# Optimization experiments

Hardware: AMD Instinct MI355X
Metric: run time of the kernel (lower is better)

## Reference

```python
import jax, jax.numpy as jnp
import numpy as np

B, T, F, L, H, O = 32, 12, 4, 1024, 64, 1  # batch, time, features, links, hidden, target features


def setup_inputs() -> dict:
    key = jax.random.key(0)
    ks = jax.random.split(key, 16)
    stdv = 1.0 / np.sqrt(H)
    u = lambda k, shape: jax.random.uniform(k, shape, jnp.float32, -stdv, stdv)
    # adjacency/attention: diagonal 1, immediate neighbors alpha=0.2 (chain road network)
    attention = jnp.eye(L, dtype=jnp.float32) \
        + 0.2 * jnp.eye(L, k=1, dtype=jnp.float32) \
        + 0.2 * jnp.eye(L, k=-1, dtype=jnp.float32)
    x = jax.random.normal(ks[0], (B, T, F, L), jnp.float32)
    return dict(
        x=x,
        attention=attention,          # [L, L] (all partitions' rows concatenated)
        w_rh=u(ks[1], (L, H, H)), b_rh=u(ks[2], (H, L)),
        w_ri=u(ks[3], (L, F, H)), b_ri=u(ks[4], (H, L)),
        w_uh=u(ks[5], (L, H, H)), b_uh=u(ks[6], (H, L)),
        w_ui=u(ks[7], (L, F, H)), b_ui=u(ks[8], (H, L)),
        w_nh=u(ks[9], (L, H, H)), b_nh=u(ks[10], (H, L)),
        w_ni=u(ks[11], (L, F, H)), b_ni=u(ks[12], (H, L)),
        w_fc=u(ks[13], (L, H, O)), b_fc=u(ks[14], (O, L)),
    )


def reference(x, attention, w_rh, b_rh, w_ri, b_ri, w_uh, b_uh, w_ui, b_ui,
              w_nh, b_nh, w_ni, b_ni, w_fc, b_fc):
    # x: [B, T, F, L]; hidden: [B, H, L]
    def step(h, xt):
        # graph attention: each link attends over its neighbors' hidden states
        hatt = jnp.einsum('bhl,pl->bhp', h, attention)  # [B, H, L]
        # per-link batched matmuls for gates
        r = jax.nn.sigmoid(
            jnp.einsum('bhl,lhk->bkl', hatt, w_rh) + b_rh[None]
            + jnp.einsum('bfl,lfk->bkl', xt, w_ri) + b_ri[None])
        z = jax.nn.sigmoid(
            jnp.einsum('bhl,lhk->bkl', hatt, w_uh) + b_uh[None]
            + jnp.einsum('bfl,lfk->bkl', xt, w_ui) + b_ui[None])
        n = jnp.tanh(
            jnp.einsum('bfl,lfk->bkl', xt, w_ni) + b_ni[None]
            + r * (jnp.einsum('bhl,lhk->bkl', hatt, w_nh) + b_nh[None]))
        h_new = (1.0 - z) * n + z * h
        return h_new, None

    h0 = jnp.zeros((B, H, L), x.dtype)
    xs = jnp.moveaxis(x, 1, 0)  # [T, B, F, L]
    hT, _ = jax.lax.scan(step, h0, xs)
    # per-link fully connected output head
    out = jnp.einsum('bhl,lht->btl', hT, w_fc) + b_fc[None]  # [B, O, L]
    return out
```

## Files before the change

### kernel.cpp

```cpp
#include <hip/hip_runtime.h>

#define B_ 32
#define T_ 12
#define F_ 4
#define L_ 1024
#define H_ 64
#define NROWS 1920
#define NCH 256
#define CONE 8
#define MARG 2

typedef _Float16 f16x8 __attribute__((ext_vector_type(8)));
typedef float f32x4 __attribute__((ext_vector_type(4)));
typedef unsigned long long u64;

#define MFMA __builtin_amdgcn_mfma_f32_16x16x32_f16

__device__ __forceinline__ int chunk_of_block(int bid) {
    return ((bid & 7) << 5) + (bid >> 3);
}
__device__ __forceinline__ int clampi(int v, int lo, int hi) {
    return v < lo ? lo : (v > hi ? hi : v);
}
__device__ __forceinline__ int h_byte(int p, int slot, int b, int k) {
    int byte = ((((p * CONE + slot) * 32 + b) * 64) + k) * 2;
    return byte ^ ((b & 7) << 4);
}

__global__ __launch_bounds__(256) void prep(
    const float* __restrict__ x,
    const float* __restrict__ b_rh, const float* __restrict__ b_ri,
    const float* __restrict__ b_uh, const float* __restrict__ b_ui,
    const float* __restrict__ b_nh, const float* __restrict__ b_ni,
    float* __restrict__ params)
{
    const int tid = threadIdx.x;
    const int rt  = blockIdx.x >> 4;
    const int lt  = blockIdx.x & 15;
    __shared__ float lds[64][65];

    #pragma unroll
    for (int i = 0; i < 16; ++i) {
        const int e  = i * 256 + tid;
        const int rl = e >> 6, ll = e & 63;
        const int r  = rt * 64 + rl, l = lt * 64 + ll;
        float v;
        if (r < 1536) {
            v = x[(size_t)r * L_ + l];
        } else {
            const int rb = r - 1536;
            const int g  = rb >> 6;
            const float* bp = (g == 0) ? b_rh : (g == 1) ? b_ri : (g == 2) ? b_uh
                            : (g == 3) ? b_ui : (g == 4) ? b_nh : b_ni;
            v = bp[(size_t)(rb & 63) * L_ + l];
        }
        lds[rl][ll] = v;
    }
    __syncthreads();
    #pragma unroll
    for (int i = 0; i < 16; ++i) {
        const int e  = i * 256 + tid;
        const int ll = e >> 6, rl = e & 63;
        params[(size_t)(lt * 64 + ll) * NROWS + rt * 64 + rl] = lds[rl][ll];
    }
}

__global__ __launch_bounds__(256) void prep_w(
    const float* __restrict__ w_rh, const float* __restrict__ w_uh,
    const float* __restrict__ w_nh,
    const float* __restrict__ w_ri, const float* __restrict__ w_ui,
    const float* __restrict__ w_ni,
    const float* __restrict__ b_rh, const float* __restrict__ b_ri,
    const float* __restrict__ b_uh, const float* __restrict__ b_ui,
    const float* __restrict__ b_ni,
    _Float16* __restrict__ Wpk)
{
    const int l  = blockIdx.x;
    const int fq = threadIdx.x >> 6, m = threadIdx.x & 63;
    const int n  = m & 15, kq = m >> 4;
    #pragma unroll
    for (int i = 0; i < 9; ++i) {
        const int f  = i * 4 + fq;
        const int nt = f / 9, s = f % 9;
        const int grp = s / 3, sub = s % 3;
        const int kout = nt * 16 + n;
        f16x8 v;
        if (sub < 2) {
            const float* wh = (grp == 0) ? w_rh : (grp == 1) ? w_uh : w_nh;
            #pragma unroll
            for (int j = 0; j < 8; ++j)
                v[j] = (_Float16)wh[(size_t)l * 4096
                         + (size_t)(sub * 32 + kq * 8 + j) * 64 + kout];
        } else {
            const float* wx = (grp == 0) ? w_ri : (grp == 1) ? w_ui : w_ni;
            float bias;
            if (grp == 0)      bias = b_rh[(size_t)kout * L_ + l] + b_ri[(size_t)kout * L_ + l];
            else if (grp == 1) bias = b_uh[(size_t)kout * L_ + l] + b_ui[(size_t)kout * L_ + l];
            else               bias = b_ni[(size_t)kout * L_ + l];
            #pragma unroll
            for (int j = 0; j < 8; ++j) {
                const int k = kq * 8 + j;
                v[j] = (k < 4) ? (_Float16)wx[(size_t)l * 256 + k * 64 + kout]
                     : (k == 4) ? (_Float16)bias
                                : (_Float16)0.0f;
            }
        }
        *(f16x8*)(Wpk + (((size_t)l * 36 + f) * 64 + m) * 8) = v;
    }
}

__global__ __launch_bounds__(512, 1) void gru_cone(
    const _Float16* __restrict__ Wpk,
    const float* __restrict__ att,  const float* __restrict__ params,
    const float* __restrict__ w_fc, const float* __restrict__ b_fc,
    float* __restrict__ out)
{
    const int c    = chunk_of_block(blockIdx.x);
    const int tid  = threadIdx.x;
    const int w    = tid >> 6, lane = tid & 63;
    const int n    = lane & 15, kq = lane >> 4;
    const int nth  = w & 1;
    const int clb  = w >> 1;
    const int base = 4 * c - MARG;

    __shared__ __align__(16) _Float16 hbuf[2 * CONE * 32 * 64];
    __shared__ __align__(16) _Float16 xls[CONE][1536];
    __shared__ float psum[4][2][B_];

    #pragma unroll
    for (int i = 0; i < 24; ++i) {
        const int e  = i * 512 + tid;
        const int cl = e / 1536, rem = e % 1536;
        const int gl = clampi(base + cl, 0, L_ - 1);
        xls[cl][rem] = (_Float16)params[(size_t)gl * NROWS + rem];
    }
    #pragma unroll
    for (int i = 0; i < 16; ++i)
        ((u64*)hbuf)[i * 512 + tid] = 0ull;

    bool     tval[2];
    _Float16 ach[2], alh[2], arh[2];
    float    bnh[2][2][4];
    f16x8    xw[2][2][3];
    #pragma unroll
    for (int j = 0; j < 2; ++j) {
        const int cl = clb + 4 * j;
        const int gl = base + cl;
        tval[j] = (gl >= 0 && gl < L_);
        const int glc = clampi(gl, 0, L_ - 1);
        ach[j] = tval[j] ? (_Float16)att[(size_t)glc * L_ + glc] : (_Float16)0.0f;
        alh[j] = (tval[j] && cl > 0 && gl > 0)
                   ? (_Float16)att[(size_t)glc * L_ + glc - 1] : (_Float16)0.0f;
        arh[j] = (tval[j] && cl < CONE - 1 && gl < L_ - 1)
                   ? (_Float16)att[(size_t)glc * L_ + glc + 1] : (_Float16)0.0f;
        const float* pb = params + (size_t)glc * NROWS + 1536;
        #pragma unroll
        for (int q = 0; q < 2; ++q) {
            #pragma unroll
            for (int r = 0; r < 4; ++r)
                bnh[j][q][r] = pb[256 + (nth * 2 + q) * 16 + kq * 4 + r];
            #pragma unroll
            for (int g = 0; g < 3; ++g)
                xw[j][q][g] = *(const f16x8*)(Wpk +
                    (((size_t)glc * 36 + (nth * 2 + q) * 9 + 2 + 3 * g) * 64 + lane) * 8);
        }
    }
    const int oidx = (clb < 2) ? clb + 2 : clb - 2;
    const int glo  = 4 * c + oidx;
    __syncthreads();

    #pragma unroll 1
    for (int t = 0; t < T_; ++t) {
        const int rp = t & 1, wpb = rp ^ 1;
        const int need = T_ - 1 - t;
        const char* hbr = (const char*)hbuf;
        char*       hbw = (char*)hbuf;

        #pragma unroll
        for (int j = 0; j < 2; ++j) {
            const int cl = clb + 4 * j;
            if (!tval[j]) continue;
            if (cl < 2 - need || cl > 5 + need) continue;
            const int gl = base + cl;
            const bool hid = (t > 0);

            f16x8 af[2][2];
            if (hid) {
                #pragma unroll
                for (int mt = 0; mt < 2; ++mt)
                    #pragma unroll
                    for (int ks = 0; ks < 2; ++ks) {
                        const int b = mt * 16 + n, k0 = ks * 32 + kq * 8;
                        const int sl = (cl > 0) ? cl - 1 : 0;
                        const int sr = (cl < CONE - 1) ? cl + 1 : CONE - 1;
                        const f16x8 hs = *(const f16x8*)(hbr + h_byte(rp, cl, b, k0));
                        const f16x8 hl = *(const f16x8*)(hbr + h_byte(rp, sl, b, k0));
                        const f16x8 hr = *(const f16x8*)(hbr + h_byte(rp, sr, b, k0));
                        af[mt][ks] = ach[j] * hs + alh[j] * hl + arh[j] * hr;
                    }
            }
            f16x8 ax[2] = {};
            if (kq == 0) {
                #pragma unroll
                for (int mt = 0; mt < 2; ++mt) {
                    #pragma unroll
                    for (int f = 0; f < 4; ++f)
                        ax[mt][f] = xls[cl][(mt * 16 + n) * 48 + t * 4 + f];
                    ax[mt][4] = (_Float16)1.0f;
                }
            }

            float sfc[2] = {0.0f, 0.0f};
            #pragma unroll
            for (int q = 0; q < 2; ++q) {
                const int kb = (nth * 2 + q) * 16 + kq * 4;
                const _Float16* wb = Wpk + (((size_t)gl * 36 + (nth * 2 + q) * 9) * 64) * 8;
                f32x4 ar[2] = {}, az[2] = {}, anh_[2] = {}, anx_[2] = {};
                if (hid) {
                    const f16x8 b0 = *(const f16x8*)(wb + (0 * 64 + lane) * 8);
                    const f16x8 b1 = *(const f16x8*)(wb + (1 * 64 + lane) * 8);
                    const f16x8 b3 = *(const f16x8*)(wb + (3 * 64 + lane) * 8);
                    const f16x8 b4 = *(const f16x8*)(wb + (4 * 64 + lane) * 8);
                    const f16x8 b6 = *(const f16x8*)(wb + (6 * 64 + lane) * 8);
                    const f16x8 b7 = *(const f16x8*)(wb + (7 * 64 + lane) * 8);
                    #pragma unroll
                    for (int mt = 0; mt < 2; ++mt) {
                        ar[mt]   = MFMA(b0, af[mt][0], ar[mt],   0, 0, 0);
                        ar[mt]   = MFMA(b1, af[mt][1], ar[mt],   0, 0, 0);
                        az[mt]   = MFMA(b3, af[mt][0], az[mt],   0, 0, 0);
                        az[mt]   = MFMA(b4, af[mt][1], az[mt],   0, 0, 0);
                        anh_[mt] = MFMA(b6, af[mt][0], anh_[mt], 0, 0, 0);
                        anh_[mt] = MFMA(b7, af[mt][1], anh_[mt], 0, 0, 0);
                    }
                }
                #pragma unroll
                for (int mt = 0; mt < 2; ++mt) {
                    ar[mt]   = MFMA(xw[j][q][0], ax[mt], ar[mt],   0, 0, 0);
                    az[mt]   = MFMA(xw[j][q][1], ax[mt], az[mt],   0, 0, 0);
                    anx_[mt] = MFMA(xw[j][q][2], ax[mt], anx_[mt], 0, 0, 0);
                }
                float4 wfc4;
                if (t == T_ - 1 && j == (clb < 2 ? 1 : 0))
                    wfc4 = *(const float4*)&w_fc[(size_t)glo * H_ + kb];
                #pragma unroll
                for (int mt = 0; mt < 2; ++mt) {
                    const int b = mt * 16 + n;
                    union { u64 u; _Float16 h[4]; } hp;
                    hp.u = hid ? *(const u64*)(hbr + h_byte(rp, cl, b, kb)) : 0ull;
                    union { u64 u; _Float16 h[4]; } hvp;
                    #pragma unroll
                    for (int r = 0; r < 4; ++r) {
                        const float pre_r = ar[mt][r];
                        const float pre_z = az[mt][r];
                        const float rg = __builtin_amdgcn_rcpf(1.0f + __expf(-pre_r));
                        const float zg = __builtin_amdgcn_rcpf(1.0f + __expf(-pre_z));
                        float npre = anx_[mt][r] + rg * (anh_[mt][r] + bnh[j][q][r]);
                        npre = fminf(fmaxf(npre, -15.0f), 15.0f);
                        const float e2 = __expf(2.0f * npre);
                        const float nn = (e2 - 1.0f) * __builtin_amdgcn_rcpf(e2 + 1.0f);
                        const float hv = (1.0f - zg) * nn + zg * (float)hp.h[r];
                        hvp.h[r] = (_Float16)hv;
                        if (t == T_ - 1) sfc[mt] += hv * (&wfc4.x)[r];
                    }
                    if (t < T_ - 1)
                        *(u64*)(hbw + h_byte(wpb, cl, b, kb)) = hvp.u;
                }
            }
            if (t == T_ - 1) {
                #pragma unroll
                for (int mt = 0; mt < 2; ++mt) {
                    float s = sfc[mt];
                    s += __shfl_xor(s, 16, 64);
                    s += __shfl_xor(s, 32, 64);
                    if (kq == 0) psum[oidx][nth][mt * 16 + n] = s;
                }
            }
        }
        __syncthreads();
    }

    if (tid < 128) {
        const int o = tid >> 5, b = tid & 31;
        const int gl = 4 * c + o;
        out[(size_t)b * L_ + gl] = psum[o][0][b] + psum[o][1][b] + b_fc[gl];
    }
}

extern "C" void kernel_launch(void* const* d_in, const int* in_sizes, int n_in,
                              void* d_out, int out_size, void* d_ws, size_t ws_size,
                              hipStream_t stream) {
    const float* x    = (const float*)d_in[0];
    const float* att  = (const float*)d_in[1];
    const float* w_rh = (const float*)d_in[2];
    const float* b_rh = (const float*)d_in[3];
    const float* w_ri = (const float*)d_in[4];
    const float* b_ri = (const float*)d_in[5];
    const float* w_uh = (const float*)d_in[6];
    const float* b_uh = (const float*)d_in[7];
    const float* w_ui = (const float*)d_in[8];
    const float* b_ui = (const float*)d_in[9];
    const float* w_nh = (const float*)d_in[10];
    const float* b_nh = (const float*)d_in[11];
    const float* w_ni = (const float*)d_in[12];
    const float* b_ni = (const float*)d_in[13];
    const float* w_fc = (const float*)d_in[14];
    const float* b_fc = (const float*)d_in[15];
    float* out = (float*)d_out;

    char* ws = (char*)d_ws;
    float*    params = (float*)ws;
    _Float16* Wpk    = (_Float16*)(ws + (8u << 20));

    prep<<<480, 256, 0, stream>>>(x, b_rh, b_ri, b_uh, b_ui, b_nh, b_ni, params);
    prep_w<<<L_, 256, 0, stream>>>(w_rh, w_uh, w_nh, w_ri, w_ui, w_ni,
                                   b_rh, b_ri, b_uh, b_ui, b_ni, Wpk);
    gru_cone<<<NCH, 512, 0, stream>>>(Wpk, att, params, w_fc, b_fc, out);
}
```

Measured before the change: 107.0 us.

## Use one wave pair per cone link and stage prep_w weights through LDS

The GRU cone kernel now launches 1024 threads, 16 waves, so each wave pair owns one of the eight cone links instead of looping over two links per wave. This doubles the parallelism per block and drops the per-wave j loop and its duplicated register state, at the cost of more waves competing for registers and the barrier. Separately, prep_w loads each link's three hidden weight matrices into shared memory with coalesced float4 reads before gathering the transposed f16 fragments, replacing strided global reads.

Result: slower. 163.1 us (+52.5%).

```diff
diff --git a/kernel.cpp b/kernel.cpp
--- a/kernel.cpp
+++ b/kernel.cpp
@@ -75,9 +75,30 @@
     const float* __restrict__ b_ni,
     _Float16* __restrict__ Wpk)
 {
-    const int l  = blockIdx.x;
-    const int fq = threadIdx.x >> 6, m = threadIdx.x & 63;
-    const int n  = m & 15, kq = m >> 4;
+    const int l   = blockIdx.x;
+    const int tid = threadIdx.x;
+    const int fq  = tid >> 6, m = tid & 63;
+    const int n   = m & 15, kq = m >> 4;
+
+    __shared__ float wst[3][64][65];
+
+    const float* whs[3] = { w_rh, w_uh, w_nh };
+    #pragma unroll
+    for (int g = 0; g < 3; ++g) {
+        const float4* src = (const float4*)(whs[g] + (size_t)l * 4096);
+        #pragma unroll
+        for (int i = 0; i < 4; ++i) {
+            const int e4 = i * 256 + tid;
+            const float4 v = src[e4];
+            const int row = e4 >> 4, col = (e4 & 15) * 4;
+            wst[g][row][col]     = v.x;
+            wst[g][row][col + 1] = v.y;
+            wst[g][row][col + 2] = v.z;
+            wst[g][row][col + 3] = v.w;
+        }
+    }
+    __syncthreads();
+
     #pragma unroll
     for (int i = 0; i < 9; ++i) {
         const int f  = i * 4 + fq;
@@ -86,11 +107,9 @@
         const int kout = nt * 16 + n;
         f16x8 v;
         if (sub < 2) {
-            const float* wh = (grp == 0) ? w_rh : (grp == 1) ? w_uh : w_nh;
             #pragma unroll
             for (int j = 0; j < 8; ++j)
-                v[j] = (_Float16)wh[(size_t)l * 4096
-                         + (size_t)(sub * 32 + kq * 8 + j) * 64 + kout];
+                v[j] = (_Float16)wst[grp][sub * 32 + kq * 8 + j][kout];
         } else {
             const float* wx = (grp == 0) ? w_ri : (grp == 1) ? w_ui : w_ni;
             float bias;
@@ -109,7 +128,7 @@
     }
 }
 
-__global__ __launch_bounds__(512, 1) void gru_cone(
+__global__ __launch_bounds__(1024, 1) void gru_cone(
     const _Float16* __restrict__ Wpk,
     const float* __restrict__ att,  const float* __restrict__ params,
     const float* __restrict__ w_fc, const float* __restrict__ b_fc,
@@ -120,7 +139,7 @@
     const int w    = tid >> 6, lane = tid & 63;
     const int n    = lane & 15, kq = lane >> 4;
     const int nth  = w & 1;
-    const int clb  = w >> 1;
+    const int cl   = w >> 1;
     const int base = 4 * c - MARG;
 
     __shared__ __align__(16) _Float16 hbuf[2 * CONE * 32 * 64];
@@ -128,45 +147,39 @@
     __shared__ float psum[4][2][B_];
 
     #pragma unroll
-    for (int i = 0; i < 24; ++i) {
-        const int e  = i * 512 + tid;
-        const int cl = e / 1536, rem = e % 1536;
-        const int gl = clampi(base + cl, 0, L_ - 1);
-        xls[cl][rem] = (_Float16)params[(size_t)gl * NROWS + rem];
-    }
-    #pragma unroll
-    for (int i = 0; i < 16; ++i)
-        ((u64*)hbuf)[i * 512 + tid] = 0ull;
-
-    bool     tval[2];
-    _Float16 ach[2], alh[2], arh[2];
-    float    bnh[2][2][4];
-    f16x8    xw[2][2][3];
-    #pragma unroll
-    for (int j = 0; j < 2; ++j) {
-        const int cl = clb + 4 * j;
-        const int gl = base + cl;
-        tval[j] = (gl >= 0 && gl < L_);
-        const int glc = clampi(gl, 0, L_ - 1);
-        ach[j] = tval[j] ? (_Float16)att[(size_t)glc * L_ + glc] : (_Float16)0.0f;
-        alh[j] = (tval[j] && cl > 0 && gl > 0)
-                   ? (_Float16)att[(size_t)glc * L_ + glc - 1] : (_Float16)0.0f;
-        arh[j] = (tval[j] && cl < CONE - 1 && gl < L_ - 1)
-                   ? (_Float16)att[(size_t)glc * L_ + glc + 1] : (_Float16)0.0f;
+    for (int i = 0; i < 12; ++i) {
+        const int e  = i * 1024 + tid;
+        const int sl = e / 1536, rem = e % 1536;
+        const int gl = clampi(base + sl, 0, L_ - 1);
+        xls[sl][rem] = (_Float16)params[(size_t)gl * NROWS + rem];
+    }
+    #pragma unroll
+    for (int i = 0; i < 8; ++i)
+        ((u64*)hbuf)[i * 1024 + tid] = 0ull;
+
+    const int  gl   = base + cl;
+    const bool tval = (gl >= 0 && gl < L_);
+    const int  glc  = clampi(gl, 0, L_ - 1);
+    const _Float16 ach = tval ? (_Float16)att[(size_t)glc * L_ + glc] : (_Float16)0.0f;
+    const _Float16 alh = (tval && cl > 0 && gl > 0)
+                           ? (_Float16)att[(size_t)glc * L_ + glc - 1] : (_Float16)0.0f;
+    const _Float16 arh = (tval && cl < CONE - 1 && gl < L_ - 1)
+                           ? (_Float16)att[(size_t)glc * L_ + glc + 1] : (_Float16)0.0f;
+    float bnh[2][4];
+    f16x8 xw[2][3];
+    {
         const float* pb = params + (size_t)glc * NROWS + 1536;
         #pragma unroll
         for (int q = 0; q < 2; ++q) {
             #pragma unroll
             for (int r = 0; r < 4; ++r)
-                bnh[j][q][r] = pb[256 + (nth * 2 + q) * 16 + kq * 4 + r];
+                bnh[q][r] = pb[256 + (nth * 2 + q) * 16 + kq * 4 + r];
             #pragma unroll
             for (int g = 0; g < 3; ++g)
-                xw[j][q][g] = *(const f16x8*)(Wpk +
+                xw[q][g] = *(const f16x8*)(Wpk +
                     (((size_t)glc * 36 + (nth * 2 + q) * 9 + 2 + 3 * g) * 64 + lane) * 8);
         }
     }
-    const int oidx = (clb < 2) ? clb + 2 : clb - 2;
-    const int glo  = 4 * c + oidx;
     __syncthreads();
 
     #pragma unroll 1
@@ -176,12 +189,7 @@
         const char* hbr = (const char*)hbuf;
         char*       hbw = (char*)hbuf;
 
-        #pragma unroll
-        for (int j = 0; j < 2; ++j) {
-            const int cl = clb + 4 * j;
-            if (!tval[j]) continue;
-            if (cl < 2 - need || cl > 5 + need) continue;
-            const int gl = base + cl;
+        if (tval && cl >= 2 - need && cl <= 5 + need) {
             const bool hid = (t > 0);
 
             f16x8 af[2][2];
@@ -196,7 +204,7 @@
                         const f16x8 hs = *(const f16x8*)(hbr + h_byte(rp, cl, b, k0));
                         const f16x8 hl = *(const f16x8*)(hbr + h_byte(rp, sl, b, k0));
                         const f16x8 hr = *(const f16x8*)(hbr + h_byte(rp, sr, b, k0));
-                        af[mt][ks] = ach[j] * hs + alh[j] * hl + arh[j] * hr;
+                        af[mt][ks] = ach * hs + alh * hl + arh * hr;
                     }
             }
             f16x8 ax[2] = {};
@@ -235,13 +243,13 @@
                 }
                 #pragma unroll
                 for (int mt = 0; mt < 2; ++mt) {
-                    ar[mt]   = MFMA(xw[j][q][0], ax[mt], ar[mt],   0, 0, 0);
-                    az[mt]   = MFMA(xw[j][q][1], ax[mt], az[mt],   0, 0, 0);
-                    anx_[mt] = MFMA(xw[j][q][2], ax[mt], anx_[mt], 0, 0, 0);
+                    ar[mt]   = MFMA(xw[q][0], ax[mt], ar[mt],   0, 0, 0);
+                    az[mt]   = MFMA(xw[q][1], ax[mt], az[mt],   0, 0, 0);
+                    anx_[mt] = MFMA(xw[q][2], ax[mt], anx_[mt], 0, 0, 0);
                 }
                 float4 wfc4;
-                if (t == T_ - 1 && j == (clb < 2 ? 1 : 0))
-                    wfc4 = *(const float4*)&w_fc[(size_t)glo * H_ + kb];
+                if (t == T_ - 1)
+                    wfc4 = *(const float4*)&w_fc[(size_t)gl * H_ + kb];
                 #pragma unroll
                 for (int mt = 0; mt < 2; ++mt) {
                     const int b = mt * 16 + n;
@@ -254,7 +262,7 @@
                         const float pre_z = az[mt][r];
                         const float rg = __builtin_amdgcn_rcpf(1.0f + __expf(-pre_r));
                         const float zg = __builtin_amdgcn_rcpf(1.0f + __expf(-pre_z));
-                        float npre = anx_[mt][r] + rg * (anh_[mt][r] + bnh[j][q][r]);
+                        float npre = anx_[mt][r] + rg * (anh_[mt][r] + bnh[q][r]);
                         npre = fminf(fmaxf(npre, -15.0f), 15.0f);
                         const float e2 = __expf(2.0f * npre);
                         const float nn = (e2 - 1.0f) * __builtin_amdgcn_rcpf(e2 + 1.0f);
@@ -272,7 +280,7 @@
                     float s = sfc[mt];
                     s += __shfl_xor(s, 16, 64);
                     s += __shfl_xor(s, 32, 64);
-                    if (kq == 0) psum[oidx][nth][mt * 16 + n] = s;
+                    if (kq == 0) psum[cl - 2][nth][mt * 16 + n] = s;
                 }
             }
         }
@@ -281,8 +289,8 @@
 
     if (tid < 128) {
         const int o = tid >> 5, b = tid & 31;
-        const int gl = 4 * c + o;
-        out[(size_t)b * L_ + gl] = psum[o][0][b] + psum[o][1][b] + b_fc[gl];
+        const int gl2 = 4 * c + o;
+        out[(size_t)b * L_ + gl2] = psum[o][0][b] + psum[o][1][b] + b_fc[gl2];
     }
 }
 
@@ -314,5 +322,5 @@
     prep<<<480, 256, 0, stream>>>(x, b_rh, b_ri, b_uh, b_ui, b_nh, b_ni, params);
     prep_w<<<L_, 256, 0, stream>>>(w_rh, w_uh, w_nh, w_ri, w_ui, w_ni,
                                    b_rh, b_ri, b_uh, b_ui, b_ni, Wpk);
-    gru_cone<<<NCH, 512, 0, stream>>>(Wpk, att, params, w_fc, b_fc, out);
-}
+    gru_cone<<<NCH, 1024, 0, stream>>>(Wpk, att, params, w_fc, b_fc, out);
+}
```

## Split batch across two blocks per chunk and stage recurrent weights in LDS

Applied to the files above, without the earlier changes.

The main GRU kernel now launches twice as many blocks, each handling 16 of the 32 batch rows for a chunk of links. This halves the per-block MFMA and LDS work and spreads it over more of the GPU's compute units, at the cost of loading each link's weights twice. Separately, prep_w now loads the recurrent weight matrices into shared memory with coalesced float4 reads before repacking them, instead of strided global gathers. The final FC reduction is also simplified so each block writes outputs only for its own half of the batch.

Result: slower. 113.5 us (+6.1%).

```diff
diff --git a/kernel.cpp b/kernel.cpp
--- a/kernel.cpp
+++ b/kernel.cpp
@@ -6,9 +6,9 @@
 #define L_ 1024
 #define H_ 64
 #define NROWS 1920
-#define NCH 256
 #define CONE 8
 #define MARG 2
+#define HB 16
 
 typedef _Float16 f16x8 __attribute__((ext_vector_type(8)));
 typedef float f32x4 __attribute__((ext_vector_type(4)));
@@ -16,14 +16,14 @@
 
 #define MFMA __builtin_amdgcn_mfma_f32_16x16x32_f16
 
-__device__ __forceinline__ int chunk_of_block(int bid) {
-    return ((bid & 7) << 5) + (bid >> 3);
+__device__ __forceinline__ int meta_of_block(int bid) {
+    return ((bid & 7) << 6) + (bid >> 3);
 }
 __device__ __forceinline__ int clampi(int v, int lo, int hi) {
     return v < lo ? lo : (v > hi ? hi : v);
 }
 __device__ __forceinline__ int h_byte(int p, int slot, int b, int k) {
-    int byte = ((((p * CONE + slot) * 32 + b) * 64) + k) * 2;
+    int byte = ((((p * CONE + slot) * HB + b) * 64) + k) * 2;
     return byte ^ ((b & 7) << 4);
 }
 
@@ -75,9 +75,30 @@
     const float* __restrict__ b_ni,
     _Float16* __restrict__ Wpk)
 {
-    const int l  = blockIdx.x;
-    const int fq = threadIdx.x >> 6, m = threadIdx.x & 63;
-    const int n  = m & 15, kq = m >> 4;
+    const int l   = blockIdx.x;
+    const int tid = threadIdx.x;
+    const int fq  = tid >> 6, m = tid & 63;
+    const int n   = m & 15, kq = m >> 4;
+
+    __shared__ float wst[3][64][65];
+
+    const float* whs[3] = { w_rh, w_uh, w_nh };
+    #pragma unroll
+    for (int g = 0; g < 3; ++g) {
+        const float4* src = (const float4*)(whs[g] + (size_t)l * 4096);
+        #pragma unroll
+        for (int i = 0; i < 4; ++i) {
+            const int e4 = i * 256 + tid;
+            const float4 v = src[e4];
+            const int row = e4 >> 4, col = (e4 & 15) * 4;
+            wst[g][row][col]     = v.x;
+            wst[g][row][col + 1] = v.y;
+            wst[g][row][col + 2] = v.z;
+            wst[g][row][col + 3] = v.w;
+        }
+    }
+    __syncthreads();
+
     #pragma unroll
     for (int i = 0; i < 9; ++i) {
         const int f  = i * 4 + fq;
@@ -86,11 +107,9 @@
         const int kout = nt * 16 + n;
         f16x8 v;
         if (sub < 2) {
-            const float* wh = (grp == 0) ? w_rh : (grp == 1) ? w_uh : w_nh;
             #pragma unroll
             for (int j = 0; j < 8; ++j)
-                v[j] = (_Float16)wh[(size_t)l * 4096
-                         + (size_t)(sub * 32 + kq * 8 + j) * 64 + kout];
+                v[j] = (_Float16)wst[grp][sub * 32 + kq * 8 + j][kout];
         } else {
             const float* wx = (grp == 0) ? w_ri : (grp == 1) ? w_ui : w_ni;
             float bias;
@@ -115,7 +134,8 @@
     const float* __restrict__ w_fc, const float* __restrict__ b_fc,
     float* __restrict__ out)
 {
-    const int c    = chunk_of_block(blockIdx.x);
+    const int meta = meta_of_block(blockIdx.x);
+    const int c    = meta >> 1, half = meta & 1;
     const int tid  = threadIdx.x;
     const int w    = tid >> 6, lane = tid & 63;
     const int n    = lane & 15, kq = lane >> 4;
@@ -123,19 +143,19 @@
     const int clb  = w >> 1;
     const int base = 4 * c - MARG;
 
-    __shared__ __align__(16) _Float16 hbuf[2 * CONE * 32 * 64];
-    __shared__ __align__(16) _Float16 xls[CONE][1536];
-    __shared__ float psum[4][2][B_];
-
-    #pragma unroll
-    for (int i = 0; i < 24; ++i) {
+    __shared__ __align__(16) _Float16 hbuf[2 * CONE * HB * 64];
+    __shared__ __align__(16) _Float16 xls[CONE][HB * 48];
+    __shared__ float psum[4][2][HB];
+
+    #pragma unroll
+    for (int i = 0; i < 12; ++i) {
         const int e  = i * 512 + tid;
-        const int cl = e / 1536, rem = e % 1536;
-        const int gl = clampi(base + cl, 0, L_ - 1);
-        xls[cl][rem] = (_Float16)params[(size_t)gl * NROWS + rem];
-    }
-    #pragma unroll
-    for (int i = 0; i < 16; ++i)
+        const int sl = e / (HB * 48), rem = e % (HB * 48);
+        const int gl = clampi(base + sl, 0, L_ - 1);
+        xls[sl][rem] = (_Float16)params[(size_t)gl * NROWS + half * (HB * 48) + rem];
+    }
+    #pragma unroll
+    for (int i = 0; i < 8; ++i)
         ((u64*)hbuf)[i * 512 + tid] = 0ull;
 
     bool     tval[2];
@@ -166,7 +186,6 @@
         }
     }
     const int oidx = (clb < 2) ? clb + 2 : clb - 2;
-    const int glo  = 4 * c + oidx;
     __syncthreads();
 
     #pragma unroll 1
@@ -184,38 +203,33 @@
             const int gl = base + cl;
             const bool hid = (t > 0);
 
-            f16x8 af[2][2];
+            f16x8 af[2];
             if (hid) {
                 #pragma unroll
-                for (int mt = 0; mt < 2; ++mt)
-                    #pragma unroll
-                    for (int ks = 0; ks < 2; ++ks) {
-                        const int b = mt * 16 + n, k0 = ks * 32 + kq * 8;
-                        const int sl = (cl > 0) ? cl - 1 : 0;
-                        const int sr = (cl < CONE - 1) ? cl + 1 : CONE - 1;
-                        const f16x8 hs = *(const f16x8*)(hbr + h_byte(rp, cl, b, k0));
-                        const f16x8 hl = *(const f16x8*)(hbr + h_byte(rp, sl, b, k0));
-                        const f16x8 hr = *(const f16x8*)(hbr + h_byte(rp, sr, b, k0));
-                        af[mt][ks] = ach[j] * hs + alh[j] * hl + arh[j] * hr;
-                    }
-            }
-            f16x8 ax[2] = {};
+                for (int ks = 0; ks < 2; ++ks) {
+                    const int k0 = ks * 32 + kq * 8;
+                    const int sl = (cl > 0) ? cl - 1 : 0;
+                    const int sr = (cl < CONE - 1) ? cl + 1 : CONE - 1;
+                    const f16x8 hs = *(const f16x8*)(hbr + h_byte(rp, cl, n, k0));
+                    const f16x8 hl = *(const f16x8*)(hbr + h_byte(rp, sl, n, k0));
+                    const f16x8 hr = *(const f16x8*)(hbr + h_byte(rp, sr, n, k0));
+                    af[ks] = ach[j] * hs + alh[j] * hl + arh[j] * hr;
+                }
+            }
+            f16x8 ax = {};
             if (kq == 0) {
                 #pragma unroll
-                for (int mt = 0; mt < 2; ++mt) {
-                    #pragma unroll
-                    for (int f = 0; f < 4; ++f)
-                        ax[mt][f] = xls[cl][(mt * 16 + n) * 48 + t * 4 + f];
-                    ax[mt][4] = (_Float16)1.0f;
-                }
-            }
-
-            float sfc[2] = {0.0f, 0.0f};
+                for (int f = 0; f < 4; ++f)
+                    ax[f] = xls[cl][n * 48 + t * 4 + f];
+                ax[4] = (_Float16)1.0f;
+            }
+
+            float sfc = 0.0f;
             #pragma unroll
             for (int q = 0; q < 2; ++q) {
                 const int kb = (nth * 2 + q) * 16 + kq * 4;
                 const _Float16* wb = Wpk + (((size_t)gl * 36 + (nth * 2 + q) * 9) * 64) * 8;
-                f32x4 ar[2] = {}, az[2] = {}, anh_[2] = {}, anx_[2] = {};
+                f32x4 ar = {}, az = {}, anh_ = {}, anx_ = {};
                 if (hid) {
                     const f16x8 b0 = *(const f16x8*)(wb + (0 * 64 + lane) * 8);
                     const f16x8 b1 = *(const f16x8*)(wb + (1 * 64 + lane) * 8);
@@ -223,66 +237,55 @@
                     const f16x8 b4 = *(const f16x8*)(wb + (4 * 64 + lane) * 8);
                     const f16x8 b6 = *(const f16x8*)(wb + (6 * 64 + lane) * 8);
                     const f16x8 b7 = *(const f16x8*)(wb + (7 * 64 + lane) * 8);
-                    #pragma unroll
-                    for (int mt = 0; mt < 2; ++mt) {
-                        ar[mt]   = MFMA(b0, af[mt][0], ar[mt],   0, 0, 0);
-                        ar[mt]   = MFMA(b1, af[mt][1], ar[mt],   0, 0, 0);
-                        az[mt]   = MFMA(b3, af[mt][0], az[mt],   0, 0, 0);
-                        az[mt]   = MFMA(b4, af[mt][1], az[mt],   0, 0, 0);
-                        anh_[mt] = MFMA(b6, af[mt][0], anh_[mt], 0, 0, 0);
-                        anh_[mt] = MFMA(b7, af[mt][1], anh_[mt], 0, 0, 0);
-                    }
+                    ar   = MFMA(b0, af[0], ar,   0, 0, 0);
+                    ar   = MFMA(b1, af[1], ar,   0, 0, 0);
+                    az   = MFMA(b3, af[0], az,   0, 0, 0);
+                    az   = MFMA(b4, af[1], az,   0, 0, 0);
+                    anh_ = MFMA(b6, af[0], anh_, 0, 0, 0);
+                    anh_ = MFMA(b7, af[1], anh_, 0, 0, 0);
                 }
+                ar   = MFMA(xw[j][q][0], ax, ar,   0, 0, 0);
+                az   = MFMA(xw[j][q][1], ax, az,   0, 0, 0);
+                anx_ = MFMA(xw[j][q][2], ax, anx_, 0, 0, 0);
+
+                float4 wfc4;
+                if (t == T_ - 1)
+                    wfc4 = *(const float4*)&w_fc[(size_t)gl * H_ + kb];
+                union { u64 u; _Float16 h[4]; } hp;
+                hp.u = hid ? *(const u64*)(hbr + h_byte(rp, cl, n, kb)) : 0ull;
+                union { u64 u; _Float16 h[4]; } hvp;
                 #pragma unroll
-                for (int mt = 0; mt < 2; ++mt) {
-                    ar[mt]   = MFMA(xw[j][q][0], ax[mt], ar[mt],   0, 0, 0);
-                    az[mt]   = MFMA(xw[j][q][1], ax[mt], az[mt],   0, 0, 0);
-                    anx_[mt] = MFMA(xw[j][q][2], ax[mt], anx_[mt], 0, 0, 0);
+                for (int r = 0; r < 4; ++r) {
+                    const float pre_r = ar[r];
+                    const float pre_z = az[r];
+                    const float rg = __builtin_amdgcn_rcpf(1.0f + __expf(-pre_r));
+                    const float zg = __builtin_amdgcn_rcpf(1.0f + __expf(-pre_z));
+                    float npre = anx_[r] + rg * (anh_[r] + bnh[j][q][r]);
+                    npre = fminf(fmaxf(npre, -15.0f), 15.0f);
+                    const float e2 = __expf(2.0f * npre);
+                    const float nn = (e2 - 1.0f) * __builtin_amdgcn_rcpf(e2 + 1.0f);
+                    const float hv = (1.0f - zg) * nn + zg * (float)hp.h[r];
+                    hvp.h[r] = (_Float16)hv;
+                    if (t == T_ - 1) sfc += hv * (&wfc4.x)[r];
                 }
-                float4 wfc4;
-                if (t == T_ - 1 && j == (clb < 2 ? 1 : 0))
-                    wfc4 = *(const float4*)&w_fc[(size_t)glo * H_ + kb];
-                #pragma unroll
-                for (int mt = 0; mt < 2; ++mt) {
-                    const int b = mt * 16 + n;
-                    union { u64 u; _Float16 h[4]; } hp;
-                    hp.u = hid ? *(const u64*)(hbr + h_byte(rp, cl, b, kb)) : 0ull;
-                    union { u64 u; _Float16 h[4]; } hvp;
-                    #pragma unroll
-                    for (int r = 0; r < 4; ++r) {
-                        const float pre_r = ar[mt][r];
-                        const float pre_z = az[mt][r];
-                        const float rg = __builtin_amdgcn_rcpf(1.0f + __expf(-pre_r));
-                        const float zg = __builtin_amdgcn_rcpf(1.0f + __expf(-pre_z));
-                        float npre = anx_[mt][r] + rg * (anh_[mt][r] + bnh[j][q][r]);
-                        npre = fminf(fmaxf(npre, -15.0f), 15.0f);
-                        const float e2 = __expf(2.0f * npre);
-                        const float nn = (e2 - 1.0f) * __builtin_amdgcn_rcpf(e2 + 1.0f);
-                        const float hv = (1.0f - zg) * nn + zg * (float)hp.h[r];
-                        hvp.h[r] = (_Float16)hv;
-                        if (t == T_ - 1) sfc[mt] += hv * (&wfc4.x)[r];
-                    }
-                    if (t < T_ - 1)
-                        *(u64*)(hbw + h_byte(wpb, cl, b, kb)) = hvp.u;
-                }
+                if (t < T_ - 1)
+                    *(u64*)(hbw + h_byte(wpb, cl, n, kb)) = hvp.u;
             }
             if (t == T_ - 1) {
-                #pragma unroll
-                for (int mt = 0; mt < 2; ++mt) {
-                    float s = sfc[mt];
-                    s += __shfl_xor(s, 16, 64);
-                    s += __shfl_xor(s, 32, 64);
-                    if (kq == 0) psum[oidx][nth][mt * 16 + n] = s;
-                }
+                float s = sfc;
+                s += __shfl_xor(s, 16, 64);
+                s += __shfl_xor(s, 32, 64);
+                if (kq == 0) psum[oidx][nth][n] = s;
             }
         }
         __syncthreads();
     }
 
-    if (tid < 128) {
-        const int o = tid >> 5, b = tid & 31;
-        const int gl = 4 * c + o;
-        out[(size_t)b * L_ + gl] = psum[o][0][b] + psum[o][1][b] + b_fc[gl];
+    if (tid < 64) {
+        const int o = tid >> 4, bl = tid & 15;
+        const int gl2 = 4 * c + o;
+        out[(size_t)(half * HB + bl) * L_ + gl2] =
+            psum[o][0][bl] + psum[o][1][bl] + b_fc[gl2];
     }
 }
 
@@ -314,5 +317,5 @@
     prep<<<480, 256, 0, stream>>>(x, b_rh, b_ri, b_uh, b_ui, b_nh, b_ni, params);
     prep_w<<<L_, 256, 0, stream>>>(w_rh, w_uh, w_nh, w_ri, w_ui, w_ni,
                                    b_rh, b_ri, b_uh, b_ui, b_ni, Wpk);
-    gru_cone<<<NCH, 512, 0, stream>>>(Wpk, att, params, w_fc, b_fc, out);
-}
+    gru_cone<<<512, 512, 0, stream>>>(Wpk, att, params, w_fc, b_fc, out);
+}
```

## Merge prep kernels, stage recurrent weights in LDS, fold log2e into weights

Applied to the files above, without the earlier changes.

Combines the two preprocessing kernels into one launch, with blocks split by index. The weight-packing path now loads each link's recurrent weight matrices into shared memory with coalesced float4 reads instead of doing strided global gathers. All gate weights and biases are pre-scaled by log2(e) or 2·log2(e), so the recurrent loop can call a native exp2 without a per-element multiply. This removes one kernel launch and some ALU work in the serial loop. The pre-scaling is applied before fp16 rounding and uses a widened clamp, which slightly changes numerics.

Result: faster. 94.81 us (-11.4%).

```diff
diff --git a/kernel.cpp b/kernel.cpp
--- a/kernel.cpp
+++ b/kernel.cpp
@@ -10,12 +10,21 @@
 #define CONE 8
 #define MARG 2
 
+#define LOG2E  1.4426950408889634f
+#define LOG2E2 2.8853900817779268f
+
 typedef _Float16 f16x8 __attribute__((ext_vector_type(8)));
 typedef float f32x4 __attribute__((ext_vector_type(4)));
 typedef unsigned long long u64;
 
 #define MFMA __builtin_amdgcn_mfma_f32_16x16x32_f16
 
+#if __has_builtin(__builtin_amdgcn_exp2f)
+#define EXP2F(x) __builtin_amdgcn_exp2f(x)
+#else
+#define EXP2F(x) __expf((x) * 0.69314718056f)
+#endif
+
 __device__ __forceinline__ int chunk_of_block(int bid) {
     return ((bid & 7) << 5) + (bid >> 3);
 }
@@ -27,70 +36,84 @@
     return byte ^ ((b & 7) << 4);
 }
 
-__global__ __launch_bounds__(256) void prep(
+__global__ __launch_bounds__(256) void prep_all(
     const float* __restrict__ x,
     const float* __restrict__ b_rh, const float* __restrict__ b_ri,
     const float* __restrict__ b_uh, const float* __restrict__ b_ui,
     const float* __restrict__ b_nh, const float* __restrict__ b_ni,
-    float* __restrict__ params)
-{
-    const int tid = threadIdx.x;
-    const int rt  = blockIdx.x >> 4;
-    const int lt  = blockIdx.x & 15;
-    __shared__ float lds[64][65];
-
-    #pragma unroll
-    for (int i = 0; i < 16; ++i) {
-        const int e  = i * 256 + tid;
-        const int rl = e >> 6, ll = e & 63;
-        const int r  = rt * 64 + rl, l = lt * 64 + ll;
-        float v;
-        if (r < 1536) {
-            v = x[(size_t)r * L_ + l];
-        } else {
-            const int rb = r - 1536;
-            const int g  = rb >> 6;
-            const float* bp = (g == 0) ? b_rh : (g == 1) ? b_ri : (g == 2) ? b_uh
-                            : (g == 3) ? b_ui : (g == 4) ? b_nh : b_ni;
-            v = bp[(size_t)(rb & 63) * L_ + l];
-        }
-        lds[rl][ll] = v;
-    }
-    __syncthreads();
-    #pragma unroll
-    for (int i = 0; i < 16; ++i) {
-        const int e  = i * 256 + tid;
-        const int ll = e >> 6, rl = e & 63;
-        params[(size_t)(lt * 64 + ll) * NROWS + rt * 64 + rl] = lds[rl][ll];
-    }
-}
-
-__global__ __launch_bounds__(256) void prep_w(
     const float* __restrict__ w_rh, const float* __restrict__ w_uh,
     const float* __restrict__ w_nh,
     const float* __restrict__ w_ri, const float* __restrict__ w_ui,
     const float* __restrict__ w_ni,
-    const float* __restrict__ b_rh, const float* __restrict__ b_ri,
-    const float* __restrict__ b_uh, const float* __restrict__ b_ui,
-    const float* __restrict__ b_ni,
-    _Float16* __restrict__ Wpk)
+    float* __restrict__ params, _Float16* __restrict__ Wpk)
 {
-    const int l  = blockIdx.x;
-    const int fq = threadIdx.x >> 6, m = threadIdx.x & 63;
+    __shared__ float sh[3][64][65];
+    const int tid = threadIdx.x;
+
+    if (blockIdx.x < 480) {
+        const int rt = blockIdx.x >> 4;
+        const int lt = blockIdx.x & 15;
+        float (*lds)[65] = sh[0];
+        #pragma unroll
+        for (int i = 0; i < 16; ++i) {
+            const int e  = i * 256 + tid;
+            const int rl = e >> 6, ll = e & 63;
+            const int r  = rt * 64 + rl, l = lt * 64 + ll;
+            float v;
+            if (r < 1536) {
+                v = x[(size_t)r * L_ + l];
+            } else {
+                const int rb = r - 1536;
+                const int g  = rb >> 6;
+                const float* bp = (g == 0) ? b_rh : (g == 1) ? b_ri : (g == 2) ? b_uh
+                                : (g == 3) ? b_ui : (g == 4) ? b_nh : b_ni;
+                v = bp[(size_t)(rb & 63) * L_ + l];
+            }
+            lds[rl][ll] = v;
+        }
+        __syncthreads();
+        #pragma unroll
+        for (int i = 0; i < 16; ++i) {
+            const int e  = i * 256 + tid;
+            const int ll = e >> 6, rl = e & 63;
+            params[(size_t)(lt * 64 + ll) * NROWS + rt * 64 + rl] = lds[rl][ll];
+        }
+        return;
+    }
+
+    const int l  = blockIdx.x - 480;
+    const int fq = tid >> 6, m = tid & 63;
     const int n  = m & 15, kq = m >> 4;
+
+    const float* whs[3] = { w_rh, w_uh, w_nh };
+    #pragma unroll
+    for (int g = 0; g < 3; ++g) {
+        const float4* src = (const float4*)(whs[g] + (size_t)l * 4096);
+        #pragma unroll
+        for (int i = 0; i < 4; ++i) {
+            const int e4 = i * 256 + tid;
+            const float4 v = src[e4];
+            const int row = e4 >> 4, col = (e4 & 15) * 4;
+            sh[g][row][col]     = v.x;
+            sh[g][row][col + 1] = v.y;
+            sh[g][row][col + 2] = v.z;
+            sh[g][row][col + 3] = v.w;
+        }
+    }
+    __syncthreads();
+
     #pragma unroll
     for (int i = 0; i < 9; ++i) {
         const int f  = i * 4 + fq;
         const int nt = f / 9, s = f % 9;
         const int grp = s / 3, sub = s % 3;
         const int kout = nt * 16 + n;
+        const float scale = (grp == 2) ? LOG2E2 : LOG2E;
         f16x8 v;
         if (sub < 2) {
-            const float* wh = (grp == 0) ? w_rh : (grp == 1) ? w_uh : w_nh;
             #pragma unroll
             for (int j = 0; j < 8; ++j)
-                v[j] = (_Float16)wh[(size_t)l * 4096
-                         + (size_t)(sub * 32 + kq * 8 + j) * 64 + kout];
+                v[j] = (_Float16)(sh[grp][sub * 32 + kq * 8 + j][kout] * scale);
         } else {
             const float* wx = (grp == 0) ? w_ri : (grp == 1) ? w_ui : w_ni;
             float bias;
@@ -100,8 +123,8 @@
             #pragma unroll
             for (int j = 0; j < 8; ++j) {
                 const int k = kq * 8 + j;
-                v[j] = (k < 4) ? (_Float16)wx[(size_t)l * 256 + k * 64 + kout]
-                     : (k == 4) ? (_Float16)bias
+                v[j] = (k < 4) ? (_Float16)(wx[(size_t)l * 256 + k * 64 + kout] * scale)
+                     : (k == 4) ? (_Float16)(bias * scale)
                                 : (_Float16)0.0f;
             }
         }
@@ -158,7 +181,7 @@
         for (int q = 0; q < 2; ++q) {
             #pragma unroll
             for (int r = 0; r < 4; ++r)
-                bnh[j][q][r] = pb[256 + (nth * 2 + q) * 16 + kq * 4 + r];
+                bnh[j][q][r] = pb[256 + (nth * 2 + q) * 16 + kq * 4 + r] * LOG2E2;
             #pragma unroll
             for (int g = 0; g < 3; ++g)
                 xw[j][q][g] = *(const f16x8*)(Wpk +
@@ -250,13 +273,11 @@
                     union { u64 u; _Float16 h[4]; } hvp;
                     #pragma unroll
                     for (int r = 0; r < 4; ++r) {
-                        const float pre_r = ar[mt][r];
-                        const float pre_z = az[mt][r];
-                        const float rg = __builtin_amdgcn_rcpf(1.0f + __expf(-pre_r));
-                        const float zg = __builtin_amdgcn_rcpf(1.0f + __expf(-pre_z));
+                        const float rg = __builtin_amdgcn_rcpf(1.0f + EXP2F(-ar[mt][r]));
+                        const float zg = __builtin_amdgcn_rcpf(1.0f + EXP2F(-az[mt][r]));
                         float npre = anx_[mt][r] + rg * (anh_[mt][r] + bnh[j][q][r]);
-                        npre = fminf(fmaxf(npre, -15.0f), 15.0f);
-                        const float e2 = __expf(2.0f * npre);
+                        npre = fminf(fmaxf(npre, -43.0f), 43.0f);
+                        const float e2 = EXP2F(npre);
                         const float nn = (e2 - 1.0f) * __builtin_amdgcn_rcpf(e2 + 1.0f);
                         const float hv = (1.0f - zg) * nn + zg * (float)hp.h[r];
                         hvp.h[r] = (_Float16)hv;
@@ -311,8 +332,8 @@
     float*    params = (float*)ws;
     _Float16* Wpk    = (_Float16*)(ws + (8u << 20));
 
-    prep<<<480, 256, 0, stream>>>(x, b_rh, b_ri, b_uh, b_ui, b_nh, b_ni, params);
-    prep_w<<<L_, 256, 0, stream>>>(w_rh, w_uh, w_nh, w_ri, w_ui, w_ni,
-                                   b_rh, b_ri, b_uh, b_ui, b_ni, Wpk);
+    prep_all<<<1504, 256, 0, stream>>>(x, b_rh, b_ri, b_uh, b_ui, b_nh, b_ni,
+                                       w_rh, w_uh, w_nh, w_ri, w_ui, w_ni,
+                                       params, Wpk);
     gru_cone<<<NCH, 512, 0, stream>>>(Wpk, att, params, w_fc, b_fc, out);
 }
```
